# Kernel optimization log

Hardware: AMD Instinct MI355X
Metric: run time of the kernel (lower is better)

The kernel has to match this reference:

```python
import jax, jax.numpy as jnp
import numpy as np

B, NQ, D, H, P, BEV, FFN = 8, 900, 256, 8, 4, 200, 512
HD = D // H
RADIUS = 0.2


def _ln(x, s, b):
    m = x.mean(-1, keepdims=True)
    v = ((x - m) ** 2).mean(-1, keepdims=True)
    return (x - m) / jnp.sqrt(v + 1e-5) * s + b


def _grid_sample(feat, grid):
    # feat: [BH, C, Hh, Ww]; grid: [BH, Q, P, 2] in [-1, 1]
    # bilinear, padding_mode='zeros', align_corners=False (matches F.grid_sample)
    BH, C, Hh, Ww = feat.shape
    gx = (grid[..., 0] + 1.0) * (Ww * 0.5) - 0.5
    gy = (grid[..., 1] + 1.0) * (Hh * 0.5) - 0.5
    x0 = jnp.floor(gx)
    y0 = jnp.floor(gy)
    wx1 = gx - x0
    wy1 = gy - y0

    def corner(xi, yi, w):
        valid = (xi >= 0) & (xi < Ww) & (yi >= 0) & (yi < Hh)
        xc = jnp.clip(xi, 0, Ww - 1).astype(jnp.int32)
        yc = jnp.clip(yi, 0, Hh - 1).astype(jnp.int32)
        vals = jax.vmap(lambda fm, yy, xx: fm[:, yy, xx])(feat, yc, xc)  # [BH, C, Q, P]
        return vals * (w * valid)[:, None, :, :]

    return (corner(x0, y0, (1 - wx1) * (1 - wy1))
            + corner(x0 + 1, y0, wx1 * (1 - wy1))
            + corner(x0, y0 + 1, (1 - wx1) * wy1)
            + corner(x0 + 1, y0 + 1, wx1 * wy1))


def _forward(query, memory, reference_points, query_pos,
             in_w, in_b, out_w, out_b,
             off_w, off_b, wt_w, wt_b, co_w, co_b,
             f_w1, f_b1, f_w2, f_b2,
             n1s, n1b, n2s, n2b, n3s, n3b, bev_h, bev_w):
    b, nq, d = query.shape
    # ---- self-attention (eval mode: dropout = identity) ----
    q_in = _ln(query + query_pos, n1s, n1b)
    qkv = q_in @ in_w.T + in_b
    q, k, v = jnp.split(qkv, 3, axis=-1)
    q = q.reshape(b, nq, H, HD)
    k = k.reshape(b, nq, H, HD)
    v = v.reshape(b, nq, H, HD)
    scores = jnp.einsum('bqhd,bkhd->bhqk', q, k) * (1.0 / HD ** 0.5)
    attn = jax.nn.softmax(scores, axis=-1)
    self_out = jnp.einsum('bhqk,bkhd->bqhd', attn, v).reshape(b, nq, d) @ out_w.T + out_b
    query = query + self_out
    # ---- deformable cross-attention over BEV memory ----
    q2 = _ln(query + query_pos, n2s, n2b)
    offsets = jnp.tanh(q2 @ off_w.T + off_b).reshape(b, nq, H, P, 2) * RADIUS
    weights = jax.nn.softmax((q2 @ wt_w.T + wt_b).reshape(b, nq, H, P), axis=-1)
    locations = reference_points[:, :, None, None, :2] + offsets  # [b, nq, H, P, 2]
    feat = memory.transpose(0, 2, 1).reshape(b * H, HD, bev_h, bev_w)
    grid = locations.transpose(0, 2, 1, 3, 4).reshape(b * H, nq, P, 2) * 2.0 - 1.0
    sampled = _grid_sample(feat, grid).reshape(b, H, HD, nq, P)
    fused = jnp.einsum('bhdqp,bqhp->bqhd', sampled, weights).reshape(b, nq, d)
    query = query + (fused @ co_w.T + co_b)
    # ---- FFN ----
    q3 = _ln(query, n3s, n3b)
    ffn = jax.nn.relu(q3 @ f_w1.T + f_b1) @ f_w2.T + f_b2
    return query + ffn


def setup_inputs() -> dict:
    key = jax.random.key(0)
    ks = jax.random.split(key, 16)
    s = 0.02
    return dict(
        query=jax.random.normal(ks[0], (B, NQ, D), jnp.float32),
        memory=jax.random.normal(ks[1], (B, BEV * BEV, D), jnp.float32),
        reference_points=jax.random.uniform(ks[2], (B, NQ, 2), jnp.float32),
        query_pos=jax.random.normal(ks[3], (B, NQ, D), jnp.float32),
        in_w=jax.random.normal(ks[4], (3 * D, D), jnp.float32) * s,
        in_b=jnp.zeros((3 * D,), jnp.float32),
        out_w=jax.random.normal(ks[5], (D, D), jnp.float32) * s,
        out_b=jnp.zeros((D,), jnp.float32),
        off_w=jax.random.normal(ks[6], (H * P * 2, D), jnp.float32) * s,
        off_b=jnp.zeros((H * P * 2,), jnp.float32),
        wt_w=jax.random.normal(ks[7], (H * P, D), jnp.float32) * s,
        wt_b=jnp.zeros((H * P,), jnp.float32),
        co_w=jax.random.normal(ks[8], (D, D), jnp.float32) * s,
        co_b=jnp.zeros((D,), jnp.float32),
        f_w1=jax.random.normal(ks[9], (FFN, D), jnp.float32) * s,
        f_b1=jnp.zeros((FFN,), jnp.float32),
        f_w2=jax.random.normal(ks[10], (D, FFN), jnp.float32) * s,
        f_b2=jnp.zeros((D,), jnp.float32),
        n1s=jnp.ones((D,), jnp.float32), n1b=jnp.zeros((D,), jnp.float32),
        n2s=jnp.ones((D,), jnp.float32), n2b=jnp.zeros((D,), jnp.float32),
        n3s=jnp.ones((D,), jnp.float32), n3b=jnp.zeros((D,), jnp.float32),
        bev_h=BEV, bev_w=BEV,
    )


def reference(query, memory, reference_points, query_pos,
              in_w, in_b, out_w, out_b,
              off_w, off_b, wt_w, wt_b, co_w, co_b,
              f_w1, f_b1, f_w2, f_b2,
              n1s, n1b, n2s, n2b, n3s, n3b, bev_h, bev_w):
    return _forward(query, memory, reference_points, query_pos,
                    in_w, in_b, out_w, out_b,
                    off_w, off_b, wt_w, wt_b, co_w, co_b,
                    f_w1, f_b1, f_w2, f_b2,
                    n1s, n1b, n2s, n2b, n3s, n3b, bev_h, bev_w)
```

## Files before the change

### kernel.cpp

```cpp
#include <hip/hip_runtime.h>
#include <math.h>

#define B_   8
#define NQ_  900
#define D_   256
#define H_   8
#define P_   4
#define BEV_ 200
#define FFN_ 512
#define HD_  32
#define M_   (B_*NQ_)
#define NKPAD 960

typedef __attribute__((ext_vector_type(8))) short short8;
typedef __attribute__((ext_vector_type(4))) float floatx4;

__device__ inline unsigned short f2bf(float f) {
    union { float f; unsigned u; } v; v.f = f;
    unsigned r = v.u + 0x7fffu + ((v.u >> 16) & 1u);
    return (unsigned short)(r >> 16);
}
__device__ inline float bf2f(unsigned short h) {
    union { unsigned u; float f; } v; v.u = ((unsigned)h) << 16;
    return v.f;
}

__global__ __launch_bounds__(256)
void prologue(const float* __restrict__ in_w, const float* __restrict__ out_w,
              const float* __restrict__ off_w, const float* __restrict__ wt_w,
              const float* __restrict__ co_w, const float* __restrict__ f_w1,
              const float* __restrict__ f_w2, const float* __restrict__ off_b,
              const float* __restrict__ wt_b,
              unsigned short* __restrict__ wb, float* __restrict__ bias_ow,
              unsigned short* __restrict__ Qb, unsigned short* __restrict__ Kb,
              unsigned short* __restrict__ Vt,
              const float* __restrict__ query, const float* __restrict__ query_pos,
              const float* __restrict__ n1s, const float* __restrict__ n1b,
              unsigned short* __restrict__ ln_out)
{
    const int bx = blockIdx.x;
    const int t  = threadIdx.x;
    if (bx < 2401) {
        int i = bx * 256 + t;
        if (i < 196608)      { wb[i] = f2bf(in_w[i]); }
        else if (i < 262144) { wb[i] = f2bf(out_w[i - 196608]); }
        else if (i < 278528) { wb[i] = f2bf(off_w[i - 262144]); }
        else if (i < 286720) { wb[i] = f2bf(wt_w[i - 278528]); }
        else if (i < 352256) { wb[i] = f2bf(co_w[i - 286720]); }
        else if (i < 483328) { wb[i] = f2bf(f_w1[i - 352256]); }
        else if (i < 614400) { wb[i] = f2bf(f_w2[i - 483328]); }
        else if (i < 614464) { bias_ow[i - 614400] = off_b[i - 614400]; }
        else if (i < 614496) { bias_ow[i - 614400] = wt_b[i - 614464]; }
    } else if (bx < 2881) {
        int j  = (bx - 2401) * 256 + t;
        int bh = j / 1920;
        int rem = j - bh * 1920;
        int q  = 900 + (rem >> 5);
        int ch = rem & 31;
        size_t idx = ((size_t)bh * NKPAD + q) * 32 + ch;
        Qb[idx] = 0;
        Kb[idx] = 0;
    } else if (bx < 3361) {
        int j  = (bx - 2881) * 256 + t;
        int bh = j / 1920;
        int rem = j - bh * 1920;
        int ch = rem / 60;
        int k  = rem - ch * 60;
        Vt[((size_t)bh * 32 + ch) * NKPAD + 900 + k] = 0;
    } else {
        int w    = t >> 6;
        int lane = t & 63;
        int row  = (bx - 3361) * 4 + w;
        size_t base = (size_t)row * D_ + lane * 4;
        float4 v = *(const float4*)(query + base);
        float4 p = *(const float4*)(query_pos + base);
        v.x += p.x; v.y += p.y; v.z += p.z; v.w += p.w;
        float s = v.x + v.y + v.z + v.w;
        float q = v.x*v.x + v.y*v.y + v.z*v.z + v.w*v.w;
        #pragma unroll
        for (int o = 1; o < 64; o <<= 1) {
            s += __shfl_xor(s, o, 64);
            q += __shfl_xor(q, o, 64);
        }
        float m   = s * (1.0f / D_);
        float var = q * (1.0f / D_) - m * m;
        float inv = rsqrtf(var + 1e-5f);
        float4 g = *(const float4*)(n1s + lane * 4);
        float4 b = *(const float4*)(n1b + lane * 4);
        ushort4 o4;
        o4.x = f2bf((v.x - m) * inv * g.x + b.x);
        o4.y = f2bf((v.y - m) * inv * g.y + b.y);
        o4.z = f2bf((v.z - m) * inv * g.z + b.z);
        o4.w = f2bf((v.w - m) * inv * g.w + b.w);
        *(ushort4*)(ln_out + base) = o4;
    }
}

__global__ __launch_bounds__(256)
void ln_kernel(const float* __restrict__ x, const float* __restrict__ pos,
               const float* __restrict__ gamma, const float* __restrict__ beta,
               unsigned short* __restrict__ out, int rows)
{
    int w    = threadIdx.x >> 6;
    int lane = threadIdx.x & 63;
    int row  = blockIdx.x * 4 + w;
    if (row >= rows) return;
    size_t base = (size_t)row * D_ + lane * 4;
    float4 v = *(const float4*)(x + base);
    if (pos) {
        float4 p = *(const float4*)(pos + base);
        v.x += p.x; v.y += p.y; v.z += p.z; v.w += p.w;
    }
    float s = v.x + v.y + v.z + v.w;
    float q = v.x*v.x + v.y*v.y + v.z*v.z + v.w*v.w;
    #pragma unroll
    for (int o = 1; o < 64; o <<= 1) {
        s += __shfl_xor(s, o, 64);
        q += __shfl_xor(q, o, 64);
    }
    float m   = s * (1.0f / D_);
    float var = q * (1.0f / D_) - m * m;
    float inv = rsqrtf(var + 1e-5f);
    float4 g = *(const float4*)(gamma + lane * 4);
    float4 b = *(const float4*)(beta  + lane * 4);
    ushort4 o4;
    o4.x = f2bf((v.x - m) * inv * g.x + b.x);
    o4.y = f2bf((v.y - m) * inv * g.y + b.y);
    o4.z = f2bf((v.z - m) * inv * g.z + b.z);
    o4.w = f2bf((v.w - m) * inv * g.w + b.w);
    *(ushort4*)(out + base) = o4;
}

template<int RELU, int OUTBF, int QKVOUT>
__global__ __launch_bounds__(256)
void gemm_mfma(const unsigned short* __restrict__ A, const unsigned short* __restrict__ W,
               const float* __restrict__ bias, const float* __restrict__ res,
               float* __restrict__ outf, unsigned short* __restrict__ outb,
               unsigned short* __restrict__ Qb, unsigned short* __restrict__ Kb,
               unsigned short* __restrict__ Vt,
               int M, int N, int K)
{
    __shared__ unsigned short As[128 * 32];
    __shared__ unsigned short Bs[128 * 32];
    const int t    = threadIdx.x;
    const int m0   = blockIdx.y * 128;
    const int n0   = blockIdx.x * 128;
    const int lane = t & 63;
    const int w    = t >> 6;
    const int wm   = (w >> 1) * 64;
    const int wn   = (w & 1) * 64;
    const int lr   = lane & 15;
    const int kq   = lane >> 4;

    floatx4 acc[4][4];
    #pragma unroll
    for (int i = 0; i < 4; ++i)
        #pragma unroll
        for (int j = 0; j < 4; ++j) acc[i][j] = (floatx4){0.f, 0.f, 0.f, 0.f};

    const int sr = t >> 1;
    const int sc = (t & 1) * 2;

    for (int k0 = 0; k0 < K; k0 += 32) {
        uint4 a0 = {0,0,0,0}, a1 = {0,0,0,0};
        int gm = m0 + sr;
        if (gm < M) {
            const uint4* src = (const uint4*)(A + (size_t)gm * K + k0 + sc * 8);
            a0 = src[0]; a1 = src[1];
        }
        *(uint4*)&As[sr * 32 + ((sc    ) ^ (sr & 3)) * 8] = a0;
        *(uint4*)&As[sr * 32 + ((sc + 1) ^ (sr & 3)) * 8] = a1;
        uint4 b0 = {0,0,0,0}, b1 = {0,0,0,0};
        int gn = n0 + sr;
        if (gn < N) {
            const uint4* src = (const uint4*)(W + (size_t)gn * K + k0 + sc * 8);
            b0 = src[0]; b1 = src[1];
        }
        *(uint4*)&Bs[sr * 32 + ((sc    ) ^ (sr & 3)) * 8] = b0;
        *(uint4*)&Bs[sr * 32 + ((sc + 1) ^ (sr & 3)) * 8] = b1;
        __syncthreads();

        short8 af[4], bfr[4];
        #pragma unroll
        for (int i = 0; i < 4; ++i) {
            int ra = wm + i * 16 + lr;
            af[i] = *(const short8*)&As[ra * 32 + (kq ^ (ra & 3)) * 8];
            int rb = wn + i * 16 + lr;
            bfr[i] = *(const short8*)&Bs[rb * 32 + (kq ^ (rb & 3)) * 8];
        }
        #pragma unroll
        for (int mi = 0; mi < 4; ++mi)
            #pragma unroll
            for (int ni = 0; ni < 4; ++ni)
                acc[mi][ni] = __builtin_amdgcn_mfma_f32_16x16x32_bf16(
                    af[mi], bfr[ni], acc[mi][ni], 0, 0, 0);
        __syncthreads();
    }

    const int rbase = kq * 4;
    #pragma unroll
    for (int ni = 0; ni < 4; ++ni) {
        int n = n0 + wn + ni * 16 + lr;
        if (n >= N) continue;
        float bv = bias[n];
        if (QKVOUT) {
            const int type = n >> 8;
            const int hh   = (n >> 5) & 7;
            const int ch   = n & 31;
            #pragma unroll
            for (int mi = 0; mi < 4; ++mi) {
                floatx4 c = acc[mi][ni];
                #pragma unroll
                for (int r = 0; r < 4; ++r) {
                    int m = m0 + wm + mi * 16 + rbase + r;
                    if (m < M) {
                        float vl = c[r] + bv;
                        int bb = m / 900;
                        int qq = m - bb * 900;
                        size_t bh = (size_t)(bb * 8 + hh);
                        if (type == 0)
                            Qb[(bh * NKPAD + qq) * 32 + ch] = f2bf(vl * 0.17677669529663687f);
                        else if (type == 1)
                            Kb[(bh * NKPAD + qq) * 32 + ch] = f2bf(vl);
                        else
                            Vt[(bh * 32 + ch) * NKPAD + qq] = f2bf(vl);
                    }
                }
            }
        } else {
            #pragma unroll
            for (int mi = 0; mi < 4; ++mi) {
                floatx4 c = acc[mi][ni];
                #pragma unroll
                for (int r = 0; r < 4; ++r) {
                    int m = m0 + wm + mi * 16 + rbase + r;
                    if (m < M) {
                        float vl = c[r] + bv;
                        if (res) vl += res[(size_t)m * N + n];
                        if (RELU) vl = fmaxf(vl, 0.f);
                        if (OUTBF) outb[(size_t)m * N + n] = f2bf(vl);
                        else       outf[(size_t)m * N + n] = vl;
                    }
                }
            }
        }
    }
}

__global__ __launch_bounds__(256)
void gemm_offwt_prep(const unsigned short* __restrict__ A, const unsigned short* __restrict__ W,
                     const float* __restrict__ bias, const float* __restrict__ refp,
                     float4* __restrict__ sx, float4* __restrict__ sy, float4* __restrict__ sw)
{
    __shared__ unsigned short As[128 * 32];
    __shared__ unsigned short Bs[128 * 32];
    __shared__ float T[128][100];
    const int t    = threadIdx.x;
    const int m0   = blockIdx.y * 128;
    const int lane = t & 63;
    const int w    = t >> 6;
    const int wm   = (w >> 1) * 64;
    const int wn   = (w & 1) * 64;
    const int lr   = lane & 15;
    const int kq   = lane >> 4;
    const int M = M_, N = 96, K = 256;

    floatx4 acc[4][4];
    #pragma unroll
    for (int i = 0; i < 4; ++i)
        #pragma unroll
        for (int j = 0; j < 4; ++j) acc[i][j] = (floatx4){0.f, 0.f, 0.f, 0.f};

    const int sr = t >> 1;
    const int sc = (t & 1) * 2;

    for (int k0 = 0; k0 < K; k0 += 32) {
        uint4 a0 = {0,0,0,0}, a1 = {0,0,0,0};
        int gm = m0 + sr;
        if (gm < M) {
            const uint4* src = (const uint4*)(A + (size_t)gm * K + k0 + sc * 8);
            a0 = src[0]; a1 = src[1];
        }
        *(uint4*)&As[sr * 32 + ((sc    ) ^ (sr & 3)) * 8] = a0;
        *(uint4*)&As[sr * 32 + ((sc + 1) ^ (sr & 3)) * 8] = a1;
        uint4 b0 = {0,0,0,0}, b1 = {0,0,0,0};
        int gn = sr;
        if (gn < N) {
            const uint4* src = (const uint4*)(W + (size_t)gn * K + k0 + sc * 8);
            b0 = src[0]; b1 = src[1];
        }
        *(uint4*)&Bs[sr * 32 + ((sc    ) ^ (sr & 3)) * 8] = b0;
        *(uint4*)&Bs[sr * 32 + ((sc + 1) ^ (sr & 3)) * 8] = b1;
        __syncthreads();

        short8 af[4], bfr[4];
        #pragma unroll
        for (int i = 0; i < 4; ++i) {
            int ra = wm + i * 16 + lr;
            af[i] = *(const short8*)&As[ra * 32 + (kq ^ (ra & 3)) * 8];
            int rb = wn + i * 16 + lr;
            bfr[i] = *(const short8*)&Bs[rb * 32 + (kq ^ (rb & 3)) * 8];
        }
        #pragma unroll
        for (int mi = 0; mi < 4; ++mi)
            #pragma unroll
            for (int ni = 0; ni < 4; ++ni)
                acc[mi][ni] = __builtin_amdgcn_mfma_f32_16x16x32_bf16(
                    af[mi], bfr[ni], acc[mi][ni], 0, 0, 0);
        __syncthreads();
    }

    const int rbase = kq * 4;
    #pragma unroll
    for (int ni = 0; ni < 4; ++ni) {
        int n = wn + ni * 16 + lr;
        if (n >= N) continue;
        float bv = bias[n];
        #pragma unroll
        for (int mi = 0; mi < 4; ++mi) {
            floatx4 c = acc[mi][ni];
            #pragma unroll
            for (int r = 0; r < 4; ++r)
                T[wm + mi * 16 + rbase + r][n] = c[r] + bv;
        }
    }
    __syncthreads();

    #pragma unroll
    for (int it = 0; it < 4; ++it) {
        int item = t + it * 256;
        int row  = item >> 3;
        int h    = item & 7;
        int gq   = m0 + row;
        if (gq >= M) continue;
        float rx = refp[gq * 2 + 0];
        float ry = refp[gq * 2 + 1];
        const float* orow = &T[row][h * 8];
        const float* wrow = &T[row][64 + h * 4];
        float gx[4], gy[4], wv[4];
        #pragma unroll
        for (int p = 0; p < 4; ++p) {
            float ox = tanhf(orow[p * 2 + 0]) * 0.2f;
            float oy = tanhf(orow[p * 2 + 1]) * 0.2f;
            gx[p] = (rx + ox) * (float)BEV_ - 0.5f;
            gy[p] = (ry + oy) * (float)BEV_ - 0.5f;
            wv[p] = wrow[p];
        }
        float mx = fmaxf(fmaxf(wv[0], wv[1]), fmaxf(wv[2], wv[3]));
        float e0 = expf(wv[0]-mx), e1 = expf(wv[1]-mx), e2 = expf(wv[2]-mx), e3 = expf(wv[3]-mx);
        float inv = 1.f / (e0 + e1 + e2 + e3);
        int idx = gq * 8 + h;
        sx[idx] = make_float4(gx[0], gx[1], gx[2], gx[3]);
        sy[idx] = make_float4(gy[0], gy[1], gy[2], gy[3]);
        sw[idx] = make_float4(e0*inv, e1*inv, e2*inv, e3*inv);
    }
}

__global__ __launch_bounds__(256)
void flash_attn(const unsigned short* __restrict__ Qb, const unsigned short* __restrict__ Kb,
                const unsigned short* __restrict__ Vt, unsigned short* __restrict__ out)
{
    __shared__ unsigned short P_lds[4][16][72];
    const int bh   = blockIdx.y;
    const int b    = bh >> 3, h = bh & 7;
    const int q0   = blockIdx.x * 64;
    const int w    = threadIdx.x >> 6;
    const int lane = threadIdx.x & 63;
    const int lr   = lane & 15;
    const int quad = lane >> 4;

    const short8 qfrag = *(const short8*)(Qb + ((size_t)bh * NKPAD + q0 + w * 16 + lr) * 32 + quad * 8);

    floatx4 O0 = (floatx4){0.f,0.f,0.f,0.f};
    floatx4 O1 = (floatx4){0.f,0.f,0.f,0.f};
    float m_i[4] = {-INFINITY, -INFINITY, -INFINITY, -INFINITY};
    float l_i[4] = {0.f, 0.f, 0.f, 0.f};

    const unsigned short* kbase_p = Kb + (size_t)bh * NKPAD * 32;
    const unsigned short* vbase_p = Vt + (size_t)bh * 32 * NKPAD;

    for (int kt = 0; kt < 15; ++kt) {
        const int kb = kt * 64;
        short8 kf[4];
        #pragma unroll
        for (int ni = 0; ni < 4; ++ni)
            kf[ni] = *(const short8*)(kbase_p + (size_t)(kb + ni * 16 + lr) * 32 + quad * 8);
        floatx4 S[4];
        #pragma unroll
        for (int ni = 0; ni < 4; ++ni)
            S[ni] = __builtin_amdgcn_mfma_f32_16x16x32_bf16(
                qfrag, kf[ni], (floatx4){0.f,0.f,0.f,0.f}, 0, 0, 0);
        if (kt == 14) {
            #pragma unroll
            for (int ni = 0; ni < 4; ++ni) {
                int key = kb + ni * 16 + lr;
                if (key >= NQ_) S[ni] = (floatx4){-1e30f, -1e30f, -1e30f, -1e30f};
            }
        }
        float rowmax[4];
        #pragma unroll
        for (int r = 0; r < 4; ++r)
            rowmax[r] = fmaxf(fmaxf(S[0][r], S[1][r]), fmaxf(S[2][r], S[3][r]));
        #pragma unroll
        for (int off = 1; off < 16; off <<= 1)
            #pragma unroll
            for (int r = 0; r < 4; ++r)
                rowmax[r] = fmaxf(rowmax[r], __shfl_xor(rowmax[r], off, 64));
        float alpha[4], rs[4];
        #pragma unroll
        for (int r = 0; r < 4; ++r) {
            float mnew = fmaxf(m_i[r], rowmax[r]);
            alpha[r] = __expf(m_i[r] - mnew);
            m_i[r] = mnew;
            rs[r] = 0.f;
        }
        #pragma unroll
        for (int ni = 0; ni < 4; ++ni) {
            #pragma unroll
            for (int r = 0; r < 4; ++r) {
                float p = __expf(S[ni][r] - m_i[r]);
                rs[r] += p;
                P_lds[w][quad * 4 + r][ni * 16 + lr] = f2bf(p);
            }
        }
        #pragma unroll
        for (int off = 1; off < 16; off <<= 1)
            #pragma unroll
            for (int r = 0; r < 4; ++r)
                rs[r] += __shfl_xor(rs[r], off, 64);
        #pragma unroll
        for (int r = 0; r < 4; ++r) {
            l_i[r] = alpha[r] * l_i[r] + rs[r];
            O0[r] *= alpha[r];
            O1[r] *= alpha[r];
        }
        asm volatile("s_waitcnt lgkmcnt(0)" ::: "memory");
        short8 pf0 = *(const short8*)&P_lds[w][lr][quad * 8];
        short8 pf1 = *(const short8*)&P_lds[w][lr][32 + quad * 8];
        short8 vf;
        vf = *(const short8*)(vbase_p + (size_t)(lr) * NKPAD + kb + quad * 8);
        O0 = __builtin_amdgcn_mfma_f32_16x16x32_bf16(pf0, vf, O0, 0, 0, 0);
        vf = *(const short8*)(vbase_p + (size_t)(lr) * NKPAD + kb + 32 + quad * 8);
        O0 = __builtin_amdgcn_mfma_f32_16x16x32_bf16(pf1, vf, O0, 0, 0, 0);
        vf = *(const short8*)(vbase_p + (size_t)(16 + lr) * NKPAD + kb + quad * 8);
        O1 = __builtin_amdgcn_mfma_f32_16x16x32_bf16(pf0, vf, O1, 0, 0, 0);
        vf = *(const short8*)(vbase_p + (size_t)(16 + lr) * NKPAD + kb + 32 + quad * 8);
        O1 = __builtin_amdgcn_mfma_f32_16x16x32_bf16(pf1, vf, O1, 0, 0, 0);
        asm volatile("s_waitcnt lgkmcnt(0)" ::: "memory");
    }
    #pragma unroll
    for (int r = 0; r < 4; ++r) {
        int q = q0 + w * 16 + quad * 4 + r;
        if (q < NQ_) {
            float inv = 1.f / l_i[r];
            size_t base = ((size_t)(b * NQ_ + q)) * D_ + h * 32;
            out[base + lr]      = f2bf(O0[r] * inv);
            out[base + 16 + lr] = f2bf(O1[r] * inv);
        }
    }
}

__global__ __launch_bounds__(256)
void sample_kernel(const float* __restrict__ mem,
                   const float4* __restrict__ sx, const float4* __restrict__ sy,
                   const float4* __restrict__ sw, unsigned short* __restrict__ fused)
{
    int tid = blockIdx.x * 256 + threadIdx.x;
    if (tid >= B_ * NQ_ * H_ * HD_) return;
    int d   = tid & 31;
    int bqh = tid >> 5;
    int h   = bqh & 7;
    int bq  = bqh >> 3;
    int b   = bq / NQ_;
    const float* mb = mem + (size_t)b * (BEV_ * BEV_) * D_ + h * HD_ + d;
    float4 X = sx[bqh], Y = sy[bqh], W = sw[bqh];
    float xs[4] = {X.x, X.y, X.z, X.w};
    float ys[4] = {Y.x, Y.y, Y.z, Y.w};
    float ws[4] = {W.x, W.y, W.z, W.w};
    float acc = 0.f;
    #pragma unroll
    for (int p = 0; p < 4; ++p) {
        float gx = xs[p], gy = ys[p];
        float x0f = floorf(gx), y0f = floorf(gy);
        int x0 = (int)x0f, y0 = (int)y0f;
        float wx1 = gx - x0f, wy1 = gy - y0f;
        float wx0 = 1.f - wx1, wy0 = 1.f - wy1;
        float s = 0.f;
        #pragma unroll
        for (int cy = 0; cy < 2; ++cy) {
            int yy = y0 + cy;
            if (yy < 0 || yy >= BEV_) continue;
            float wyv = cy ? wy1 : wy0;
            #pragma unroll
            for (int cx = 0; cx < 2; ++cx) {
                int xx = x0 + cx;
                if (xx < 0 || xx >= BEV_) continue;
                float wxv = cx ? wx1 : wx0;
                s += wyv * wxv * mb[((size_t)yy * BEV_ + xx) * D_];
            }
        }
        acc += ws[p] * s;
    }
    fused[(size_t)bq * D_ + h * HD_ + d] = f2bf(acc);
}

extern "C" void kernel_launch(void* const* d_in, const int* in_sizes, int n_in,
                              void* d_out, int out_size, void* d_ws, size_t ws_size,
                              hipStream_t stream) {
    const float* query     = (const float*)d_in[0];
    const float* memory    = (const float*)d_in[1];
    const float* refp      = (const float*)d_in[2];
    const float* query_pos = (const float*)d_in[3];
    const float* in_w  = (const float*)d_in[4];
    const float* in_b  = (const float*)d_in[5];
    const float* out_w = (const float*)d_in[6];
    const float* out_b = (const float*)d_in[7];
    const float* off_w = (const float*)d_in[8];
    const float* off_b = (const float*)d_in[9];
    const float* wt_w  = (const float*)d_in[10];
    const float* wt_b  = (const float*)d_in[11];
    const float* co_w  = (const float*)d_in[12];
    const float* co_b  = (const float*)d_in[13];
    const float* f_w1  = (const float*)d_in[14];
    const float* f_b1  = (const float*)d_in[15];
    const float* f_w2  = (const float*)d_in[16];
    const float* f_b2  = (const float*)d_in[17];
    const float* n1s = (const float*)d_in[18];
    const float* n1b = (const float*)d_in[19];
    const float* n2s = (const float*)d_in[20];
    const float* n2b = (const float*)d_in[21];
    const float* n3s = (const float*)d_in[22];
    const float* n3b = (const float*)d_in[23];
    float* outp = (float*)d_out;

    char* w = (char*)d_ws;
    unsigned short* wb      = (unsigned short*)w;
    float*          bias_ow = (float*)(w + 1228800);
    unsigned short* ln_bf   = (unsigned short*)(w + 1229184);
    float*          q1      = (float*)(w + 4915584);
    unsigned short* Qb      = (unsigned short*)(w + 23347584);
    unsigned short* Kb      = (unsigned short*)(w + 27279744);
    unsigned short* Vt      = (unsigned short*)(w + 31211904);
    float*          samp    = (float*)(w + 15053184);
    unsigned short* fuse_bf = (unsigned short*)(w + 17817984);
    unsigned short* h1_bf   = (unsigned short*)(w + 12288384);
    unsigned short* attn_bf = ln_bf;

    const unsigned short* wb_in  = wb;
    const unsigned short* wb_out = wb + 196608;
    const unsigned short* wb_ow  = wb + 262144;
    const unsigned short* wb_co  = wb + 286720;
    const unsigned short* wb_f1  = wb + 352256;
    const unsigned short* wb_f2  = wb + 483328;

    dim3 blk(256);
    const int M = M_;

    prologue<<<dim3(5161), blk, 0, stream>>>(
        in_w, out_w, off_w, wt_w, co_w, f_w1, f_w2, off_b, wt_b, wb, bias_ow,
        Qb, Kb, Vt, query, query_pos, n1s, n1b, ln_bf);
    gemm_mfma<0,0,1><<<dim3(6, 57), blk, 0, stream>>>(ln_bf, wb_in, in_b, nullptr,
                                                      nullptr, nullptr, Qb, Kb, Vt,
                                                      M, 768, 256);
    flash_attn<<<dim3(15, 64), blk, 0, stream>>>(Qb, Kb, Vt, attn_bf);
    gemm_mfma<0,0,0><<<dim3(2, 57), blk, 0, stream>>>(attn_bf, wb_out, out_b, query,
                                                      q1, nullptr, nullptr, nullptr, nullptr,
                                                      M, 256, 256);
    ln_kernel<<<dim3(M / 4), blk, 0, stream>>>(q1, query_pos, n2s, n2b, ln_bf, M);
    gemm_offwt_prep<<<dim3(1, 57), blk, 0, stream>>>(
        ln_bf, wb_ow, bias_ow, refp,
        (float4*)samp, (float4*)samp + 57600, (float4*)samp + 115200);
    sample_kernel<<<dim3(B_ * NQ_ * H_ * HD_ / 256), blk, 0, stream>>>(
        memory, (const float4*)samp, (const float4*)samp + 57600,
        (const float4*)samp + 115200, fuse_bf);
    gemm_mfma<0,0,0><<<dim3(2, 57), blk, 0, stream>>>(fuse_bf, wb_co, co_b, q1,
                                                      outp, nullptr, nullptr, nullptr, nullptr,
                                                      M, 256, 256);
    ln_kernel<<<dim3(M / 4), blk, 0, stream>>>(outp, nullptr, n3s, n3b, ln_bf, M);
    gemm_mfma<1,1,0><<<dim3(4, 57), blk, 0, stream>>>(ln_bf, wb_f1, f_b1, nullptr,
                                                      nullptr, h1_bf, nullptr, nullptr, nullptr,
                                                      M, 512, 256);
    gemm_mfma<0,0,0><<<dim3(2, 57), blk, 0, stream>>>(h1_bf, wb_f2, f_b2, outp,
                                                      outp, nullptr, nullptr, nullptr, nullptr,
                                                      M, 256, 512);
}
```

Baseline: 663.7 us.

## Software-prefetch next K tiles in GEMMs and flash attention, double-buffer P

Both GEMM kernels now load the next K-slice of A and W into registers right after the barrier, so the global loads overlap with the MFMA work on the current slice. In flash attention, the next K tile is prefetched into registers, the V fragments are issued early, and the P scratch in LDS is double-buffered so the trailing lgkmcnt wait can be dropped. The goal is to hide global-memory latency in the inner loops. The cost is extra register pressure, which could lower occupancy.

```diff
diff --git a/kernel.cpp b/kernel.cpp
--- a/kernel.cpp
+++ b/kernel.cpp
@@ -160,25 +160,39 @@
 
     const int sr = t >> 1;
     const int sc = (t & 1) * 2;
+    const int gm = m0 + sr;
+    const int gn = n0 + sr;
+    const bool am = gm < M;
+    const bool bn = gn < N;
+
+    uint4 a0 = {0,0,0,0}, a1 = {0,0,0,0}, b0 = {0,0,0,0}, b1 = {0,0,0,0};
+    if (am) {
+        const uint4* src = (const uint4*)(A + (size_t)gm * K + sc * 8);
+        a0 = src[0]; a1 = src[1];
+    }
+    if (bn) {
+        const uint4* src = (const uint4*)(W + (size_t)gn * K + sc * 8);
+        b0 = src[0]; b1 = src[1];
+    }
 
     for (int k0 = 0; k0 < K; k0 += 32) {
-        uint4 a0 = {0,0,0,0}, a1 = {0,0,0,0};
-        int gm = m0 + sr;
-        if (gm < M) {
-            const uint4* src = (const uint4*)(A + (size_t)gm * K + k0 + sc * 8);
-            a0 = src[0]; a1 = src[1];
-        }
         *(uint4*)&As[sr * 32 + ((sc    ) ^ (sr & 3)) * 8] = a0;
         *(uint4*)&As[sr * 32 + ((sc + 1) ^ (sr & 3)) * 8] = a1;
-        uint4 b0 = {0,0,0,0}, b1 = {0,0,0,0};
-        int gn = n0 + sr;
-        if (gn < N) {
-            const uint4* src = (const uint4*)(W + (size_t)gn * K + k0 + sc * 8);
-            b0 = src[0]; b1 = src[1];
-        }
         *(uint4*)&Bs[sr * 32 + ((sc    ) ^ (sr & 3)) * 8] = b0;
         *(uint4*)&Bs[sr * 32 + ((sc + 1) ^ (sr & 3)) * 8] = b1;
         __syncthreads();
+
+        if (k0 + 32 < K) {
+            a0 = (uint4){0,0,0,0}; a1 = a0; b0 = a0; b1 = a0;
+            if (am) {
+                const uint4* src = (const uint4*)(A + (size_t)gm * K + (k0 + 32) + sc * 8);
+                a0 = src[0]; a1 = src[1];
+            }
+            if (bn) {
+                const uint4* src = (const uint4*)(W + (size_t)gn * K + (k0 + 32) + sc * 8);
+                b0 = src[0]; b1 = src[1];
+            }
+        }
 
         short8 af[4], bfr[4];
         #pragma unroll
@@ -273,25 +287,39 @@
 
     const int sr = t >> 1;
     const int sc = (t & 1) * 2;
+    const int gm = m0 + sr;
+    const int gn = sr;
+    const bool am = gm < M;
+    const bool bn = gn < N;
+
+    uint4 a0 = {0,0,0,0}, a1 = {0,0,0,0}, b0 = {0,0,0,0}, b1 = {0,0,0,0};
+    if (am) {
+        const uint4* src = (const uint4*)(A + (size_t)gm * K + sc * 8);
+        a0 = src[0]; a1 = src[1];
+    }
+    if (bn) {
+        const uint4* src = (const uint4*)(W + (size_t)gn * K + sc * 8);
+        b0 = src[0]; b1 = src[1];
+    }
 
     for (int k0 = 0; k0 < K; k0 += 32) {
-        uint4 a0 = {0,0,0,0}, a1 = {0,0,0,0};
-        int gm = m0 + sr;
-        if (gm < M) {
-            const uint4* src = (const uint4*)(A + (size_t)gm * K + k0 + sc * 8);
-            a0 = src[0]; a1 = src[1];
-        }
         *(uint4*)&As[sr * 32 + ((sc    ) ^ (sr & 3)) * 8] = a0;
         *(uint4*)&As[sr * 32 + ((sc + 1) ^ (sr & 3)) * 8] = a1;
-        uint4 b0 = {0,0,0,0}, b1 = {0,0,0,0};
-        int gn = sr;
-        if (gn < N) {
-            const uint4* src = (const uint4*)(W + (size_t)gn * K + k0 + sc * 8);
-            b0 = src[0]; b1 = src[1];
-        }
         *(uint4*)&Bs[sr * 32 + ((sc    ) ^ (sr & 3)) * 8] = b0;
         *(uint4*)&Bs[sr * 32 + ((sc + 1) ^ (sr & 3)) * 8] = b1;
         __syncthreads();
+
+        if (k0 + 32 < K) {
+            a0 = (uint4){0,0,0,0}; a1 = a0; b0 = a0; b1 = a0;
+            if (am) {
+                const uint4* src = (const uint4*)(A + (size_t)gm * K + (k0 + 32) + sc * 8);
+                a0 = src[0]; a1 = src[1];
+            }
+            if (bn) {
+                const uint4* src = (const uint4*)(W + (size_t)gn * K + (k0 + 32) + sc * 8);
+                b0 = src[0]; b1 = src[1];
+            }
+        }
 
         short8 af[4], bfr[4];
         #pragma unroll
@@ -360,7 +388,7 @@
 void flash_attn(const unsigned short* __restrict__ Qb, const unsigned short* __restrict__ Kb,
                 const unsigned short* __restrict__ Vt, unsigned short* __restrict__ out)
 {
-    __shared__ unsigned short P_lds[4][16][72];
+    __shared__ unsigned short P_lds[4][2][16][72];
     const int bh   = blockIdx.y;
     const int b    = bh >> 3, h = bh & 7;
     const int q0   = blockIdx.x * 64;
@@ -379,17 +407,27 @@
     const unsigned short* kbase_p = Kb + (size_t)bh * NKPAD * 32;
     const unsigned short* vbase_p = Vt + (size_t)bh * 32 * NKPAD;
 
+    short8 kf[4], kfn[4];
+    #pragma unroll
+    for (int ni = 0; ni < 4; ++ni)
+        kf[ni] = *(const short8*)(kbase_p + (size_t)(ni * 16 + lr) * 32 + quad * 8);
+
     for (int kt = 0; kt < 15; ++kt) {
         const int kb = kt * 64;
-        short8 kf[4];
-        #pragma unroll
-        for (int ni = 0; ni < 4; ++ni)
-            kf[ni] = *(const short8*)(kbase_p + (size_t)(kb + ni * 16 + lr) * 32 + quad * 8);
         floatx4 S[4];
         #pragma unroll
         for (int ni = 0; ni < 4; ++ni)
             S[ni] = __builtin_amdgcn_mfma_f32_16x16x32_bf16(
                 qfrag, kf[ni], (floatx4){0.f,0.f,0.f,0.f}, 0, 0, 0);
+        if (kt < 14) {
+            #pragma unroll
+            for (int ni = 0; ni < 4; ++ni)
+                kfn[ni] = *(const short8*)(kbase_p + (size_t)(kb + 64 + ni * 16 + lr) * 32 + quad * 8);
+        }
+        short8 vf0 = *(const short8*)(vbase_p + (size_t)(lr) * NKPAD + kb + quad * 8);
+        short8 vf1 = *(const short8*)(vbase_p + (size_t)(lr) * NKPAD + kb + 32 + quad * 8);
+        short8 vf2 = *(const short8*)(vbase_p + (size_t)(16 + lr) * NKPAD + kb + quad * 8);
+        short8 vf3 = *(const short8*)(vbase_p + (size_t)(16 + lr) * NKPAD + kb + 32 + quad * 8);
         if (kt == 14) {
             #pragma unroll
             for (int ni = 0; ni < 4; ++ni) {
@@ -414,13 +452,14 @@
             m_i[r] = mnew;
             rs[r] = 0.f;
         }
+        const int buf = kt & 1;
         #pragma unroll
         for (int ni = 0; ni < 4; ++ni) {
             #pragma unroll
             for (int r = 0; r < 4; ++r) {
                 float p = __expf(S[ni][r] - m_i[r]);
                 rs[r] += p;
-                P_lds[w][quad * 4 + r][ni * 16 + lr] = f2bf(p);
+                P_lds[w][buf][quad * 4 + r][ni * 16 + lr] = f2bf(p);
             }
         }
         #pragma unroll
@@ -435,18 +474,16 @@
             O1[r] *= alpha[r];
         }
         asm volatile("s_waitcnt lgkmcnt(0)" ::: "memory");
-        short8 pf0 = *(const short8*)&P_lds[w][lr][quad * 8];
-        short8 pf1 = *(const short8*)&P_lds[w][lr][32 + quad * 8];
-        short8 vf;
-        vf = *(const short8*)(vbase_p + (size_t)(lr) * NKPAD + kb + quad * 8);
-        O0 = __builtin_amdgcn_mfma_f32_16x16x32_bf16(pf0, vf, O0, 0, 0, 0);
-        vf = *(const short8*)(vbase_p + (size_t)(lr) * NKPAD + kb + 32 + quad * 8);
-        O0 = __builtin_amdgcn_mfma_f32_16x16x32_bf16(pf1, vf, O0, 0, 0, 0);
-        vf = *(const short8*)(vbase_p + (size_t)(16 + lr) * NKPAD + kb + quad * 8);
-        O1 = __builtin_amdgcn_mfma_f32_16x16x32_bf16(pf0, vf, O1, 0, 0, 0);
-        vf = *(const short8*)(vbase_p + (size_t)(16 + lr) * NKPAD + kb + 32 + quad * 8);
-        O1 = __builtin_amdgcn_mfma_f32_16x16x32_bf16(pf1, vf, O1, 0, 0, 0);
-        asm volatile("s_waitcnt lgkmcnt(0)" ::: "memory");
+        short8 pf0 = *(const short8*)&P_lds[w][buf][lr][quad * 8];
+        short8 pf1 = *(const short8*)&P_lds[w][buf][lr][32 + quad * 8];
+        O0 = __builtin_amdgcn_mfma_f32_16x16x32_bf16(pf0, vf0, O0, 0, 0, 0);
+        O0 = __builtin_amdgcn_mfma_f32_16x16x32_bf16(pf1, vf1, O0, 0, 0, 0);
+        O1 = __builtin_amdgcn_mfma_f32_16x16x32_bf16(pf0, vf2, O1, 0, 0, 0);
+        O1 = __builtin_amdgcn_mfma_f32_16x16x32_bf16(pf1, vf3, O1, 0, 0, 0);
+        if (kt < 14) {
+            #pragma unroll
+            for (int ni = 0; ni < 4; ++ni) kf[ni] = kfn[ni];
+        }
     }
     #pragma unroll
     for (int r = 0; r < 4; ++r) {
```

New measurement: 659.3 us. About the same (-0.7%).
